# Optimization experiments

Hardware: AMD Instinct MI355X
Metric: run time of the kernel (lower is better)

## Reference

```python
import jax, jax.numpy as jnp
import numpy as np

DIM = 64   # voxel grid resolution per axis
C = 64     # channels (C_in == num_outputs, required by residual add)
N = 200000 # number of points
EPS = 1e-3 # keras BatchNormalization default epsilon

def _bn(x, g, b, m, v):
    # inference-mode batch norm
    return (x - m) * jax.lax.rsqrt(v + EPS) * g + b

def _conv3d_relu(x, k, b):
    # x: [1,X,Y,Z,Cin], k: [3,3,3,Cin,Cout] (DHWIO), 'same' padding, relu activation
    y = jax.lax.conv_general_dilated(x, k, (1, 1, 1), 'SAME',
        dimension_numbers=('NDHWC', 'DHWIO', 'NDHWC'))
    return jax.nn.relu(y + b)

def _trilinear(grid, pts):
    # grid: [X,Y,Z,C], pts: [N,3] in voxel coordinates
    dmax = jnp.asarray(grid.shape[:3], pts.dtype) - 1.0
    p = jnp.clip(pts, 0.0, dmax)
    f = jnp.floor(p)
    t = p - f  # [N,3] fractional part
    i0 = f.astype(jnp.int32)
    i1 = jnp.minimum(i0 + 1, jnp.asarray(grid.shape[:3], jnp.int32) - 1)
    out = jnp.zeros((pts.shape[0], grid.shape[-1]), grid.dtype)
    for dx in (0, 1):
        for dy in (0, 1):
            for dz in (0, 1):
                ix = i1[:, 0] if dx else i0[:, 0]
                iy = i1[:, 1] if dy else i0[:, 1]
                iz = i1[:, 2] if dz else i0[:, 2]
                w = ((t[:, 0] if dx else 1.0 - t[:, 0])
                     * (t[:, 1] if dy else 1.0 - t[:, 1])
                     * (t[:, 2] if dz else 1.0 - t[:, 2]))
                out = out + w[:, None] * grid[ix, iy, iz]
    return out

def setup_inputs():
    key = jax.random.key(0)
    ks = jax.random.split(key, 10)
    inputs = jax.random.normal(ks[0], (N, C), jnp.float32)
    # pt_coords already scaled into voxel space (VOXEL_SIZE_INV folded in)
    pt_coords = jax.random.uniform(ks[1], (N, 3), jnp.float32) * (DIM - 1)
    voxel_indexes = jax.random.randint(ks[2], (N, 3), 0, DIM)
    pts_per_voxel_inv = jax.random.uniform(ks[3], (1, DIM, DIM, DIM, 1), jnp.float32)
    s = 1.0 / np.sqrt(C)
    w_mlp = jax.random.normal(ks[4], (C, C), jnp.float32) * s
    b_mlp = jnp.zeros((C,), jnp.float32)
    sk = 1.0 / np.sqrt(27 * C)
    k1 = jax.random.normal(ks[5], (3, 3, 3, C, C), jnp.float32) * sk
    cb1 = jnp.zeros((C,), jnp.float32)
    k2 = jax.random.normal(ks[6], (3, 3, 3, C, C), jnp.float32) * sk
    cb2 = jnp.zeros((C,), jnp.float32)
    def bn_params(k):
        a, b_, c = jax.random.split(k, 3)
        g = 1.0 + 0.1 * jax.random.normal(a, (C,), jnp.float32)
        be = 0.1 * jax.random.normal(b_, (C,), jnp.float32)
        m = 0.1 * jax.random.normal(c, (C,), jnp.float32)
        v = jnp.ones((C,), jnp.float32)
        return g, be, m, v
    g0, be0, m0, v0 = bn_params(ks[7])
    g1, be1, m1, v1 = bn_params(ks[8])
    g2, be2, m2, v2 = bn_params(ks[9])
    return dict(inputs=inputs, pt_coords=pt_coords, voxel_indexes=voxel_indexes,
                pts_per_voxel_inv=pts_per_voxel_inv, w_mlp=w_mlp, b_mlp=b_mlp,
                g0=g0, be0=be0, m0=m0, v0=v0, k1=k1, cb1=cb1, g1=g1, be1=be1,
                m1=m1, v1=v1, k2=k2, cb2=cb2, g2=g2, be2=be2, m2=m2, v2=v2)

def reference(inputs, pt_coords, voxel_indexes, pts_per_voxel_inv, w_mlp, b_mlp,
              g0, be0, m0, v0, k1, cb1, g1, be1, m1, v1, k2, cb2, g2, be2, m2, v2):
    # point branch: Dense(relu) + BN
    mlp_out = _bn(jax.nn.relu(inputs @ w_mlp + b_mlp), g0, be0, m0, v0)
    # voxelize: scatter_nd adds duplicate-index contributions
    voxels = jnp.zeros((DIM, DIM, DIM, C), inputs.dtype).at[
        voxel_indexes[:, 0], voxel_indexes[:, 1], voxel_indexes[:, 2]].add(inputs)
    voxels = voxels[None] * pts_per_voxel_inv  # per-voxel mean normalization
    # voxel branch: two Conv3D(relu)+BN
    h = _bn(_conv3d_relu(voxels, k1, cb1), g1, be1, m1, v1)
    h = _bn(_conv3d_relu(h, k2, cb2), g2, be2, m2, v2)
    # devoxelize: trilinear gather back to points (coords already in voxel space)
    vox_out = _trilinear(h[0], pt_coords)
    return mlp_out + vox_out
```

## Files before the change

### kernel.cpp

```cpp
#include <hip/hip_runtime.h>
#include <hip/hip_bf16.h>

#define DIMV 64
#define CH 64
#define EPSB 1e-3f

using bf16x8 = __attribute__((ext_vector_type(8))) short;
using f32x16 = __attribute__((ext_vector_type(16))) float;

__device__ __forceinline__ unsigned short f2bf(float f) {
    union { float f; unsigned u; } x; x.f = f;
    unsigned r = x.u + 0x7fff + ((x.u >> 16) & 1);
    return (unsigned short)(r >> 16);
}
__device__ __forceinline__ float bf2f(unsigned short u) {
    union { unsigned u; float f; } x; x.u = ((unsigned)u) << 16;
    return x.f;
}

__global__ void scatter_kernel(const float* __restrict__ x, const int* __restrict__ idx,
                               float* __restrict__ grid, int n_total) {
    int tid = blockIdx.x * blockDim.x + threadIdx.x;
    if (tid >= n_total) return;
    int n = tid >> 6, c = tid & 63;
    int ix = idx[n * 3 + 0], iy = idx[n * 3 + 1], iz = idx[n * 3 + 2];
    atomicAdd(&grid[(size_t)(((ix * DIMV) + iy) * DIMV + iz) * CH + c], x[tid]);
}

__global__ void pack_kernel(const float* __restrict__ A, const float* __restrict__ inv,
                            unsigned short* __restrict__ G1) {
    int t = blockIdx.x * 256 + threadIdx.x;
    if (t >= (DIMV * DIMV * DIMV * CH) / 8) return;
    int v = t >> 3, c8 = (t & 7) * 8;
    const float* src = A + (size_t)v * CH + c8;
    float s = inv[v];
    __align__(16) unsigned short tmp[8];
#pragma unroll
    for (int j = 0; j < 8; ++j) tmp[j] = f2bf(src[j] * s);
    *(int4*)(G1 + (size_t)t * 8) = *(const int4*)tmp;
}

__global__ void wprep_kernel(const float* __restrict__ K, unsigned short* __restrict__ wbuf) {
    int t = blockIdx.x * 256 + threadIdx.x;
    if (t >= 27 * 4 * 2 * 64 * 8) return;
    int j = t & 7;
    int l = (t >> 3) & 63;
    int nt = (t >> 9) & 1;
    int kkl = (t >> 10) & 3;
    int d = t >> 12;
    int ci = kkl * 16 + (l >> 5) * 8 + j;
    int co = nt * 32 + (l & 31);
    wbuf[t] = f2bf(K[((size_t)d * 64 + ci) * 64 + co]);
}

__global__ void wprep_mlp(const float* __restrict__ W, unsigned short* __restrict__ wm) {
    int t = blockIdx.x * 256 + threadIdx.x;
    if (t >= 4 * 2 * 64 * 8) return;
    int j = t & 7;
    int l = (t >> 3) & 63;
    int nt = (t >> 9) & 1;
    int kkl = (t >> 10) & 3;
    int ci = kkl * 16 + (l >> 5) * 8 + j;
    int co = nt * 32 + (l & 31);
    wm[t] = f2bf(W[(size_t)ci * 64 + co]);
}

__global__ __launch_bounds__(512) void conv_mfma(
    const unsigned short* __restrict__ G, const unsigned short* __restrict__ wbuf,
    const float* __restrict__ cb, const float* __restrict__ g,
    const float* __restrict__ be, const float* __restrict__ m,
    const float* __restrict__ v, unsigned short* __restrict__ out) {
    __shared__ __align__(16) unsigned short slab[612 * 128];
    const int tid = threadIdx.x;
    const int lane = tid & 63;
    const int w = tid >> 6;
    const int cx = w >> 1;
    const int cy0 = 2 * (w & 1);
    const int lz = lane & 31;
    const int kg = lane >> 5;
    const int BX = blockIdx.x, BY = blockIdx.y, BZ = blockIdx.z;
    const int x0 = 4 * BX - 1, y0 = 4 * BY - 1;
    const int zbase = 32 * BZ - 1;

    for (int it = 0; it < 20; ++it) {
        int idx = it * 512 + tid;
        if (idx < 9792) {
            int s = idx & 15;
            int r = idx >> 4;
            int zp = r % 17;
            int ryx = r / 17;
            int xx = x0 + ryx / 6;
            int yy = y0 + ryx % 6;
            int cp = s ^ (zp & 15);
            int c = cp >> 1, p = cp & 1;
            int zz = zbase + 2 * zp + p;
            int4 val = make_int4(0, 0, 0, 0);
            if ((unsigned)xx < DIMV && (unsigned)yy < DIMV && (unsigned)zz < DIMV)
                val = *(const int4*)(G + (size_t)(((xx * DIMV) + yy) * DIMV + zz) * CH + c * 8);
            *(int4*)(slab + (size_t)idx * 8) = val;
        }
    }
    __syncthreads();

    f32x16 acc[2][2];
#pragma unroll
    for (int ct = 0; ct < 2; ++ct)
#pragma unroll
        for (int nt = 0; nt < 2; ++nt)
#pragma unroll
            for (int r = 0; r < 16; ++r) acc[ct][nt][r] = 0.f;

    bf16x8 bfr0[8], bfr1[8];
#pragma unroll
    for (int q = 0; q < 8; ++q)
        bfr0[q] = *(const bf16x8*)(wbuf + q * 512 + lane * 8);

#pragma unroll
    for (int d = 0; d < 27; ++d) {
        if (d < 26) {
            const unsigned short* wn = wbuf + (size_t)(d + 1) * 4096;
            if (d & 1) {
#pragma unroll
                for (int q = 0; q < 8; ++q) bfr0[q] = *(const bf16x8*)(wn + q * 512 + lane * 8);
            } else {
#pragma unroll
                for (int q = 0; q < 8; ++q) bfr1[q] = *(const bf16x8*)(wn + q * 512 + lane * 8);
            }
        }
        const int dx = d / 9, dy = (d / 3) % 3, dz = d % 3;
        const int zval = lz + dz;
        const int zp = zval >> 1, p = zval & 1;
        const int rbase = ((cx + dx) * 6 + (cy0 + dy)) * 17 + zp;
#pragma unroll
        for (int kkl = 0; kkl < 4; ++kkl) {
            const int c = kkl * 2 + kg;
            const int slot = (c * 2 + p) ^ (zp & 15);
            bf16x8 a0 = *(const bf16x8*)(slab + rbase * 128 + slot * 8);
            bf16x8 a1 = *(const bf16x8*)(slab + (rbase + 17) * 128 + slot * 8);
            bf16x8 b0 = (d & 1) ? bfr1[kkl * 2 + 0] : bfr0[kkl * 2 + 0];
            bf16x8 b1 = (d & 1) ? bfr1[kkl * 2 + 1] : bfr0[kkl * 2 + 1];
            acc[0][0] = __builtin_amdgcn_mfma_f32_32x32x16_bf16(a0, b0, acc[0][0], 0, 0, 0);
            acc[1][0] = __builtin_amdgcn_mfma_f32_32x32x16_bf16(a1, b0, acc[1][0], 0, 0, 0);
            acc[0][1] = __builtin_amdgcn_mfma_f32_32x32x16_bf16(a0, b1, acc[0][1], 0, 0, 0);
            acc[1][1] = __builtin_amdgcn_mfma_f32_32x32x16_bf16(a1, b1, acc[1][1], 0, 0, 0);
        }
    }

    const int x_out = 4 * BX + cx;
#pragma unroll
    for (int ct = 0; ct < 2; ++ct) {
        int y_out = 4 * BY + cy0 + ct;
#pragma unroll
        for (int nt = 0; nt < 2; ++nt) {
            int co = nt * 32 + lz;
            float scale = g[co] * rsqrtf(v[co] + EPSB);
            float shift = be[co] - m[co] * scale;
            float bias = cb[co];
            size_t base = (size_t)((x_out * DIMV) + y_out) * DIMV * CH + co;
#pragma unroll
            for (int r = 0; r < 16; ++r) {
                int zrow = (r & 3) + 8 * (r >> 2) + 4 * kg;
                int z = BZ * 32 + zrow;
                float val = fmaxf(acc[ct][nt][r] + bias, 0.f) * scale + shift;
                out[base + (size_t)z * CH] = f2bf(val);
            }
        }
    }
}

__global__ __launch_bounds__(256) void mlp_gather(
    const float* __restrict__ x, const unsigned short* __restrict__ wfrag,
    const float* __restrict__ b, const float* __restrict__ g,
    const float* __restrict__ be, const float* __restrict__ m,
    const float* __restrict__ v, const unsigned short* __restrict__ grid,
    const float* __restrict__ pts, float* __restrict__ out, int npts) {
    __shared__ float lds[128 * 64];
    const int w = threadIdx.x >> 6;
    const int lane = threadIdx.x & 63;
    const int col = lane & 31;
    const int kg = lane >> 5;
    const int p0 = (blockIdx.x * 4 + w) * 32;

    if (p0 < npts) {
        bf16x8 a[4];
        const float* xr = x + (size_t)(p0 + col) * CH + kg * 8;
#pragma unroll
        for (int kk = 0; kk < 4; ++kk) {
            const float* p = xr + kk * 16;
            bf16x8 t;
#pragma unroll
            for (int j = 0; j < 8; ++j) t[j] = (short)f2bf(p[j]);
            a[kk] = t;
        }
        f32x16 acc[2];
#pragma unroll
        for (int nt = 0; nt < 2; ++nt)
#pragma unroll
            for (int r = 0; r < 16; ++r) acc[nt][r] = 0.f;
#pragma unroll
        for (int kk = 0; kk < 4; ++kk) {
            bf16x8 b0 = *(const bf16x8*)(wfrag + (kk * 2 + 0) * 512 + lane * 8);
            bf16x8 b1 = *(const bf16x8*)(wfrag + (kk * 2 + 1) * 512 + lane * 8);
            acc[0] = __builtin_amdgcn_mfma_f32_32x32x16_bf16(a[kk], b0, acc[0], 0, 0, 0);
            acc[1] = __builtin_amdgcn_mfma_f32_32x32x16_bf16(a[kk], b1, acc[1], 0, 0, 0);
        }
#pragma unroll
        for (int nt = 0; nt < 2; ++nt) {
            int co = nt * 32 + col;
            float scale = g[co] * rsqrtf(v[co] + EPSB);
            float shift = be[co] - m[co] * scale;
            float bias = b[co];
#pragma unroll
            for (int r = 0; r < 16; ++r) {
                int row = (r & 3) + 8 * (r >> 2) + 4 * kg;
                float val = fmaxf(acc[nt][r] + bias, 0.f) * scale + shift;
                lds[(w * 32 + row) * 64 + co] = val;
            }
        }
    }
    __syncthreads();

    const int pblk = blockIdx.x * 128;
#pragma unroll 4
    for (int i = 0; i < 32; ++i) {
        int idx = i * 256 + threadIdx.x;
        int pl = idx >> 6;
        int c = idx & 63;
        int pt = pblk + pl;
        if (pt >= npts) break;
        float px = fminf(fmaxf(pts[pt * 3 + 0], 0.f), (float)(DIMV - 1));
        float py = fminf(fmaxf(pts[pt * 3 + 1], 0.f), (float)(DIMV - 1));
        float pz = fminf(fmaxf(pts[pt * 3 + 2], 0.f), (float)(DIMV - 1));
        float fx = floorf(px), fy = floorf(py), fz = floorf(pz);
        float tx = px - fx, ty = py - fy, tz = pz - fz;
        int x0 = (int)fx, y0 = (int)fy, z0 = (int)fz;
        int x1 = min(x0 + 1, DIMV - 1), y1 = min(y0 + 1, DIMV - 1), z1 = min(z0 + 1, DIMV - 1);
        float wx0 = 1.f - tx, wy0 = 1.f - ty, wz0 = 1.f - tz;
        float acc = lds[pl * 64 + c];
        acc = fmaf(wx0 * wy0 * wz0, bf2f(grid[(size_t)(((x0 * DIMV) + y0) * DIMV + z0) * CH + c]), acc);
        acc = fmaf(wx0 * wy0 * tz,  bf2f(grid[(size_t)(((x0 * DIMV) + y0) * DIMV + z1) * CH + c]), acc);
        acc = fmaf(wx0 * ty * wz0,  bf2f(grid[(size_t)(((x0 * DIMV) + y1) * DIMV + z0) * CH + c]), acc);
        acc = fmaf(wx0 * ty * tz,   bf2f(grid[(size_t)(((x0 * DIMV) + y1) * DIMV + z1) * CH + c]), acc);
        acc = fmaf(tx * wy0 * wz0,  bf2f(grid[(size_t)(((x1 * DIMV) + y0) * DIMV + z0) * CH + c]), acc);
        acc = fmaf(tx * wy0 * tz,   bf2f(grid[(size_t)(((x1 * DIMV) + y0) * DIMV + z1) * CH + c]), acc);
        acc = fmaf(tx * ty * wz0,   bf2f(grid[(size_t)(((x1 * DIMV) + y1) * DIMV + z0) * CH + c]), acc);
        acc = fmaf(tx * ty * tz,    bf2f(grid[(size_t)(((x1 * DIMV) + y1) * DIMV + z1) * CH + c]), acc);
        out[(size_t)pt * CH + c] = acc;
    }
}

extern "C" void kernel_launch(void* const* d_in, const int* in_sizes, int n_in,
                              void* d_out, int out_size, void* d_ws, size_t ws_size,
                              hipStream_t stream) {
    const float* inputs = (const float*)d_in[0];
    const float* pt_coords = (const float*)d_in[1];
    const int* voxel_indexes = (const int*)d_in[2];
    const float* ppvi = (const float*)d_in[3];
    const float* w_mlp = (const float*)d_in[4];
    const float* b_mlp = (const float*)d_in[5];
    const float* g0 = (const float*)d_in[6];
    const float* be0 = (const float*)d_in[7];
    const float* m0 = (const float*)d_in[8];
    const float* v0 = (const float*)d_in[9];
    const float* k1 = (const float*)d_in[10];
    const float* cb1 = (const float*)d_in[11];
    const float* g1 = (const float*)d_in[12];
    const float* be1 = (const float*)d_in[13];
    const float* m1 = (const float*)d_in[14];
    const float* v1 = (const float*)d_in[15];
    const float* k2 = (const float*)d_in[16];
    const float* cb2 = (const float*)d_in[17];
    const float* g2 = (const float*)d_in[18];
    const float* be2 = (const float*)d_in[19];
    const float* m2 = (const float*)d_in[20];
    const float* v2 = (const float*)d_in[21];
    float* out = (float*)d_out;

    char* ws = (char*)d_ws;
    float* A = (float*)ws;
    unsigned short* G2 = (unsigned short*)ws;
    unsigned short* G3 = (unsigned short*)(ws + 33554432);
    unsigned short* G1 = (unsigned short*)(ws + 67108864);
    unsigned short* wbuf1 = (unsigned short*)(ws + 100663296);
    unsigned short* wbuf2 = (unsigned short*)(ws + 100884480);
    unsigned short* wmlp = (unsigned short*)(ws + 101105664);

    const int n_total = in_sizes[0];
    const int npts = n_total / CH;
    const int nblk = (n_total + 255) / 256;
    const size_t grid_elems = (size_t)DIMV * DIMV * DIMV * CH;

    hipMemsetAsync(A, 0, grid_elems * sizeof(float), stream);
    wprep_mlp<<<16, 256, 0, stream>>>(w_mlp, wmlp);
    wprep_kernel<<<432, 256, 0, stream>>>(k1, wbuf1);
    wprep_kernel<<<432, 256, 0, stream>>>(k2, wbuf2);
    scatter_kernel<<<nblk, 256, 0, stream>>>(inputs, voxel_indexes, A, n_total);
    pack_kernel<<<(int)(grid_elems / 8 + 255) / 256, 256, 0, stream>>>(A, ppvi, G1);

    dim3 cgrid(16, 16, 2);
    conv_mfma<<<cgrid, 512, 0, stream>>>(G1, wbuf1, cb1, g1, be1, m1, v1, G2);
    conv_mfma<<<cgrid, 512, 0, stream>>>(G2, wbuf2, cb2, g2, be2, m2, v2, G3);

    mlp_gather<<<(npts + 127) / 128, 256, 0, stream>>>(
        inputs, wmlp, b_mlp, g0, be0, m0, v0, G3, pt_coords, out, npts);
}
```

Measured before the change: 283.4 us.

## Fuse voxel normalize/pack into first conv and reuse A fragments across dy

Removes the separate pack kernel: the first conv now reads the fp32 scatter grid, scales by the per-voxel inverse count and converts to bf16 while filling shared memory. The conv block shrinks to 4 waves, each computing a full 4-row y strip so each loaded A fragment serves up to three dy taps, and weights are loaded directly per tap instead of double-buffered across taps. This aims to remove a full grid round trip and cut LDS reads, at the cost of more registers (8 accumulators), half the threads per block for the same slab fill, and uncoalesced fp32 reads in the fused fill.

```diff
diff --git a/kernel.cpp b/kernel.cpp
--- a/kernel.cpp
+++ b/kernel.cpp
@@ -25,19 +25,6 @@
     int n = tid >> 6, c = tid & 63;
     int ix = idx[n * 3 + 0], iy = idx[n * 3 + 1], iz = idx[n * 3 + 2];
     atomicAdd(&grid[(size_t)(((ix * DIMV) + iy) * DIMV + iz) * CH + c], x[tid]);
-}
-
-__global__ void pack_kernel(const float* __restrict__ A, const float* __restrict__ inv,
-                            unsigned short* __restrict__ G1) {
-    int t = blockIdx.x * 256 + threadIdx.x;
-    if (t >= (DIMV * DIMV * DIMV * CH) / 8) return;
-    int v = t >> 3, c8 = (t & 7) * 8;
-    const float* src = A + (size_t)v * CH + c8;
-    float s = inv[v];
-    __align__(16) unsigned short tmp[8];
-#pragma unroll
-    for (int j = 0; j < 8; ++j) tmp[j] = f2bf(src[j] * s);
-    *(int4*)(G1 + (size_t)t * 8) = *(const int4*)tmp;
 }
 
 __global__ void wprep_kernel(const float* __restrict__ K, unsigned short* __restrict__ wbuf) {
@@ -65,8 +52,10 @@
     wm[t] = f2bf(W[(size_t)ci * 64 + co]);
 }
 
-__global__ __launch_bounds__(512) void conv_mfma(
-    const unsigned short* __restrict__ G, const unsigned short* __restrict__ wbuf,
+template <int FUSE>
+__global__ __launch_bounds__(256) void conv_mfma(
+    const unsigned short* __restrict__ Gb, const float* __restrict__ Gf,
+    const float* __restrict__ inv, const unsigned short* __restrict__ wbuf,
     const float* __restrict__ cb, const float* __restrict__ g,
     const float* __restrict__ be, const float* __restrict__ m,
     const float* __restrict__ v, unsigned short* __restrict__ out) {
@@ -74,16 +63,14 @@
     const int tid = threadIdx.x;
     const int lane = tid & 63;
     const int w = tid >> 6;
-    const int cx = w >> 1;
-    const int cy0 = 2 * (w & 1);
     const int lz = lane & 31;
     const int kg = lane >> 5;
     const int BX = blockIdx.x, BY = blockIdx.y, BZ = blockIdx.z;
     const int x0 = 4 * BX - 1, y0 = 4 * BY - 1;
     const int zbase = 32 * BZ - 1;
 
-    for (int it = 0; it < 20; ++it) {
-        int idx = it * 512 + tid;
+    for (int it = 0; it < 39; ++it) {
+        int idx = it * 256 + tid;
         if (idx < 9792) {
             int s = idx & 15;
             int r = idx >> 4;
@@ -94,62 +81,72 @@
             int cp = s ^ (zp & 15);
             int c = cp >> 1, p = cp & 1;
             int zz = zbase + 2 * zp + p;
-            int4 val = make_int4(0, 0, 0, 0);
-            if ((unsigned)xx < DIMV && (unsigned)yy < DIMV && (unsigned)zz < DIMV)
-                val = *(const int4*)(G + (size_t)(((xx * DIMV) + yy) * DIMV + zz) * CH + c * 8);
-            *(int4*)(slab + (size_t)idx * 8) = val;
+            if (FUSE) {
+                __align__(16) unsigned short tmp[8] = {0, 0, 0, 0, 0, 0, 0, 0};
+                if ((unsigned)xx < DIMV && (unsigned)yy < DIMV && (unsigned)zz < DIMV) {
+                    int vox = ((xx * DIMV) + yy) * DIMV + zz;
+                    const float* src = Gf + (size_t)vox * CH + c * 8;
+                    float sc = inv[vox];
+#pragma unroll
+                    for (int j = 0; j < 8; ++j) tmp[j] = f2bf(src[j] * sc);
+                }
+                *(int4*)(slab + (size_t)idx * 8) = *(const int4*)tmp;
+            } else {
+                int4 val = make_int4(0, 0, 0, 0);
+                if ((unsigned)xx < DIMV && (unsigned)yy < DIMV && (unsigned)zz < DIMV)
+                    val = *(const int4*)(Gb + (size_t)(((xx * DIMV) + yy) * DIMV + zz) * CH + c * 8);
+                *(int4*)(slab + (size_t)idx * 8) = val;
+            }
         }
     }
     __syncthreads();
 
-    f32x16 acc[2][2];
-#pragma unroll
-    for (int ct = 0; ct < 2; ++ct)
+    f32x16 acc[4][2];
+#pragma unroll
+    for (int yc = 0; yc < 4; ++yc)
 #pragma unroll
         for (int nt = 0; nt < 2; ++nt)
 #pragma unroll
-            for (int r = 0; r < 16; ++r) acc[ct][nt][r] = 0.f;
-
-    bf16x8 bfr0[8], bfr1[8];
-#pragma unroll
-    for (int q = 0; q < 8; ++q)
-        bfr0[q] = *(const bf16x8*)(wbuf + q * 512 + lane * 8);
-
-#pragma unroll
-    for (int d = 0; d < 27; ++d) {
-        if (d < 26) {
-            const unsigned short* wn = wbuf + (size_t)(d + 1) * 4096;
-            if (d & 1) {
-#pragma unroll
-                for (int q = 0; q < 8; ++q) bfr0[q] = *(const bf16x8*)(wn + q * 512 + lane * 8);
-            } else {
-#pragma unroll
-                for (int q = 0; q < 8; ++q) bfr1[q] = *(const bf16x8*)(wn + q * 512 + lane * 8);
+            for (int r = 0; r < 16; ++r) acc[yc][nt][r] = 0.f;
+
+#pragma unroll
+    for (int dx = 0; dx < 3; ++dx)
+#pragma unroll
+        for (int dz = 0; dz < 3; ++dz) {
+            const int zval = lz + dz;
+            const int zp = zval >> 1, p = zval & 1;
+            const int rb = ((w + dx) * 6) * 17 + zp;
+#pragma unroll
+            for (int kkl = 0; kkl < 4; ++kkl) {
+                const int slot = ((kkl * 2 + kg) * 2 + p) ^ (zp & 15);
+                bf16x8 a[6];
+#pragma unroll
+                for (int ys = 0; ys < 6; ++ys)
+                    a[ys] = *(const bf16x8*)(slab + (rb + ys * 17) * 128 + slot * 8);
+                bf16x8 bb[3][2];
+#pragma unroll
+                for (int dy = 0; dy < 3; ++dy) {
+                    const unsigned short* wd =
+                        wbuf + (size_t)(dx * 9 + dy * 3 + dz) * 4096 + (kkl * 2) * 512 + lane * 8;
+                    bb[dy][0] = *(const bf16x8*)(wd);
+                    bb[dy][1] = *(const bf16x8*)(wd + 512);
+                }
+#pragma unroll
+                for (int dy = 0; dy < 3; ++dy)
+#pragma unroll
+                    for (int yc = 0; yc < 4; ++yc) {
+                        acc[yc][0] = __builtin_amdgcn_mfma_f32_32x32x16_bf16(
+                            a[yc + dy], bb[dy][0], acc[yc][0], 0, 0, 0);
+                        acc[yc][1] = __builtin_amdgcn_mfma_f32_32x32x16_bf16(
+                            a[yc + dy], bb[dy][1], acc[yc][1], 0, 0, 0);
+                    }
             }
         }
-        const int dx = d / 9, dy = (d / 3) % 3, dz = d % 3;
-        const int zval = lz + dz;
-        const int zp = zval >> 1, p = zval & 1;
-        const int rbase = ((cx + dx) * 6 + (cy0 + dy)) * 17 + zp;
-#pragma unroll
-        for (int kkl = 0; kkl < 4; ++kkl) {
-            const int c = kkl * 2 + kg;
-            const int slot = (c * 2 + p) ^ (zp & 15);
-            bf16x8 a0 = *(const bf16x8*)(slab + rbase * 128 + slot * 8);
-            bf16x8 a1 = *(const bf16x8*)(slab + (rbase + 17) * 128 + slot * 8);
-            bf16x8 b0 = (d & 1) ? bfr1[kkl * 2 + 0] : bfr0[kkl * 2 + 0];
-            bf16x8 b1 = (d & 1) ? bfr1[kkl * 2 + 1] : bfr0[kkl * 2 + 1];
-            acc[0][0] = __builtin_amdgcn_mfma_f32_32x32x16_bf16(a0, b0, acc[0][0], 0, 0, 0);
-            acc[1][0] = __builtin_amdgcn_mfma_f32_32x32x16_bf16(a1, b0, acc[1][0], 0, 0, 0);
-            acc[0][1] = __builtin_amdgcn_mfma_f32_32x32x16_bf16(a0, b1, acc[0][1], 0, 0, 0);
-            acc[1][1] = __builtin_amdgcn_mfma_f32_32x32x16_bf16(a1, b1, acc[1][1], 0, 0, 0);
-        }
-    }
-
-    const int x_out = 4 * BX + cx;
-#pragma unroll
-    for (int ct = 0; ct < 2; ++ct) {
-        int y_out = 4 * BY + cy0 + ct;
+
+    const int x_out = 4 * BX + w;
+#pragma unroll
+    for (int yc = 0; yc < 4; ++yc) {
+        int y_out = 4 * BY + yc;
 #pragma unroll
         for (int nt = 0; nt < 2; ++nt) {
             int co = nt * 32 + lz;
@@ -161,7 +158,7 @@
             for (int r = 0; r < 16; ++r) {
                 int zrow = (r & 3) + 8 * (r >> 2) + 4 * kg;
                 int z = BZ * 32 + zrow;
-                float val = fmaxf(acc[ct][nt][r] + bias, 0.f) * scale + shift;
+                float val = fmaxf(acc[yc][nt][r] + bias, 0.f) * scale + shift;
                 out[base + (size_t)z * CH] = f2bf(val);
             }
         }
@@ -278,9 +275,8 @@
 
     char* ws = (char*)d_ws;
     float* A = (float*)ws;
-    unsigned short* G2 = (unsigned short*)ws;
-    unsigned short* G3 = (unsigned short*)(ws + 33554432);
-    unsigned short* G1 = (unsigned short*)(ws + 67108864);
+    unsigned short* G3 = (unsigned short*)ws;
+    unsigned short* G2 = (unsigned short*)(ws + 67108864);
     unsigned short* wbuf1 = (unsigned short*)(ws + 100663296);
     unsigned short* wbuf2 = (unsigned short*)(ws + 100884480);
     unsigned short* wmlp = (unsigned short*)(ws + 101105664);
@@ -295,11 +291,10 @@
     wprep_kernel<<<432, 256, 0, stream>>>(k1, wbuf1);
     wprep_kernel<<<432, 256, 0, stream>>>(k2, wbuf2);
     scatter_kernel<<<nblk, 256, 0, stream>>>(inputs, voxel_indexes, A, n_total);
-    pack_kernel<<<(int)(grid_elems / 8 + 255) / 256, 256, 0, stream>>>(A, ppvi, G1);
 
     dim3 cgrid(16, 16, 2);
-    conv_mfma<<<cgrid, 512, 0, stream>>>(G1, wbuf1, cb1, g1, be1, m1, v1, G2);
-    conv_mfma<<<cgrid, 512, 0, stream>>>(G2, wbuf2, cb2, g2, be2, m2, v2, G3);
+    conv_mfma<1><<<cgrid, 256, 0, stream>>>(nullptr, A, ppvi, wbuf1, cb1, g1, be1, m1, v1, G2);
+    conv_mfma<0><<<cgrid, 256, 0, stream>>>(G2, nullptr, nullptr, wbuf2, cb2, g2, be2, m2, v2, G3);
 
     mlp_gather<<<(npts + 127) / 128, 256, 0, stream>>>(
         inputs, wmlp, b_mlp, g0, be0, m0, v0, G3, pt_coords, out, npts);
```

Measured after the change: 301.9 us. 6.5% more time.

## Fuse voxel normalization and bf16 packing into first conv, add MFMA priority

Applied to the files above, without the earlier changes.

Removes the separate pack kernel: the first conv now reads the fp32 scatter grid directly, scales by the per-voxel inverse count and converts to bf16 while filling its shared-memory slab. This drops one full-grid write and read pass plus a launch. The cost is that the halo voxels are read twice as much data (fp32) and converted redundantly across blocks. It also raises wave priority around the MFMA loop via s_setprio and reshuffles the workspace buffers.

```diff
diff --git a/kernel.cpp b/kernel.cpp
--- a/kernel.cpp
+++ b/kernel.cpp
@@ -25,19 +25,6 @@
     int n = tid >> 6, c = tid & 63;
     int ix = idx[n * 3 + 0], iy = idx[n * 3 + 1], iz = idx[n * 3 + 2];
     atomicAdd(&grid[(size_t)(((ix * DIMV) + iy) * DIMV + iz) * CH + c], x[tid]);
-}
-
-__global__ void pack_kernel(const float* __restrict__ A, const float* __restrict__ inv,
-                            unsigned short* __restrict__ G1) {
-    int t = blockIdx.x * 256 + threadIdx.x;
-    if (t >= (DIMV * DIMV * DIMV * CH) / 8) return;
-    int v = t >> 3, c8 = (t & 7) * 8;
-    const float* src = A + (size_t)v * CH + c8;
-    float s = inv[v];
-    __align__(16) unsigned short tmp[8];
-#pragma unroll
-    for (int j = 0; j < 8; ++j) tmp[j] = f2bf(src[j] * s);
-    *(int4*)(G1 + (size_t)t * 8) = *(const int4*)tmp;
 }
 
 __global__ void wprep_kernel(const float* __restrict__ K, unsigned short* __restrict__ wbuf) {
@@ -65,8 +52,10 @@
     wm[t] = f2bf(W[(size_t)ci * 64 + co]);
 }
 
+template <int FUSE>
 __global__ __launch_bounds__(512) void conv_mfma(
-    const unsigned short* __restrict__ G, const unsigned short* __restrict__ wbuf,
+    const unsigned short* __restrict__ Gb, const float* __restrict__ Gf,
+    const float* __restrict__ inv, const unsigned short* __restrict__ wbuf,
     const float* __restrict__ cb, const float* __restrict__ g,
     const float* __restrict__ be, const float* __restrict__ m,
     const float* __restrict__ v, unsigned short* __restrict__ out) {
@@ -94,10 +83,22 @@
             int cp = s ^ (zp & 15);
             int c = cp >> 1, p = cp & 1;
             int zz = zbase + 2 * zp + p;
-            int4 val = make_int4(0, 0, 0, 0);
-            if ((unsigned)xx < DIMV && (unsigned)yy < DIMV && (unsigned)zz < DIMV)
-                val = *(const int4*)(G + (size_t)(((xx * DIMV) + yy) * DIMV + zz) * CH + c * 8);
-            *(int4*)(slab + (size_t)idx * 8) = val;
+            if (FUSE) {
+                __align__(16) unsigned short tmp[8] = {0, 0, 0, 0, 0, 0, 0, 0};
+                if ((unsigned)xx < DIMV && (unsigned)yy < DIMV && (unsigned)zz < DIMV) {
+                    int vox = ((xx * DIMV) + yy) * DIMV + zz;
+                    const float* src = Gf + (size_t)vox * CH + c * 8;
+                    float sc = inv[vox];
+#pragma unroll
+                    for (int j = 0; j < 8; ++j) tmp[j] = f2bf(src[j] * sc);
+                }
+                *(int4*)(slab + (size_t)idx * 8) = *(const int4*)tmp;
+            } else {
+                int4 val = make_int4(0, 0, 0, 0);
+                if ((unsigned)xx < DIMV && (unsigned)yy < DIMV && (unsigned)zz < DIMV)
+                    val = *(const int4*)(Gb + (size_t)(((xx * DIMV) + yy) * DIMV + zz) * CH + c * 8);
+                *(int4*)(slab + (size_t)idx * 8) = val;
+            }
         }
     }
     __syncthreads();
@@ -131,6 +132,7 @@
         const int zval = lz + dz;
         const int zp = zval >> 1, p = zval & 1;
         const int rbase = ((cx + dx) * 6 + (cy0 + dy)) * 17 + zp;
+        __builtin_amdgcn_s_setprio(1);
 #pragma unroll
         for (int kkl = 0; kkl < 4; ++kkl) {
             const int c = kkl * 2 + kg;
@@ -144,6 +146,7 @@
             acc[0][1] = __builtin_amdgcn_mfma_f32_32x32x16_bf16(a0, b1, acc[0][1], 0, 0, 0);
             acc[1][1] = __builtin_amdgcn_mfma_f32_32x32x16_bf16(a1, b1, acc[1][1], 0, 0, 0);
         }
+        __builtin_amdgcn_s_setprio(0);
     }
 
     const int x_out = 4 * BX + cx;
@@ -278,9 +281,8 @@
 
     char* ws = (char*)d_ws;
     float* A = (float*)ws;
-    unsigned short* G2 = (unsigned short*)ws;
-    unsigned short* G3 = (unsigned short*)(ws + 33554432);
-    unsigned short* G1 = (unsigned short*)(ws + 67108864);
+    unsigned short* G3 = (unsigned short*)ws;
+    unsigned short* G2 = (unsigned short*)(ws + 67108864);
     unsigned short* wbuf1 = (unsigned short*)(ws + 100663296);
     unsigned short* wbuf2 = (unsigned short*)(ws + 100884480);
     unsigned short* wmlp = (unsigned short*)(ws + 101105664);
@@ -295,11 +297,10 @@
     wprep_kernel<<<432, 256, 0, stream>>>(k1, wbuf1);
     wprep_kernel<<<432, 256, 0, stream>>>(k2, wbuf2);
     scatter_kernel<<<nblk, 256, 0, stream>>>(inputs, voxel_indexes, A, n_total);
-    pack_kernel<<<(int)(grid_elems / 8 + 255) / 256, 256, 0, stream>>>(A, ppvi, G1);
 
     dim3 cgrid(16, 16, 2);
-    conv_mfma<<<cgrid, 512, 0, stream>>>(G1, wbuf1, cb1, g1, be1, m1, v1, G2);
-    conv_mfma<<<cgrid, 512, 0, stream>>>(G2, wbuf2, cb2, g2, be2, m2, v2, G3);
+    conv_mfma<1><<<cgrid, 512, 0, stream>>>(nullptr, A, ppvi, wbuf1, cb1, g1, be1, m1, v1, G2);
+    conv_mfma<0><<<cgrid, 512, 0, stream>>>(G2, nullptr, nullptr, wbuf2, cb2, g2, be2, m2, v2, G3);
 
     mlp_gather<<<(npts + 127) / 128, 256, 0, stream>>>(
         inputs, wmlp, b_mlp, g0, be0, m0, v0, G3, pt_coords, out, npts);
```

Result: no change. 279.3 us (-1.5%).
